# Kernel tuning notes

Measured on AMD Instinct MI355X. Metric: run time of the kernel, lower is better.

The kernel has to match this reference:

```python
import jax, jax.numpy as jnp
import numpy as np

D_MODEL = 1024
N_HEADS = 16
D_K = 64
BATCH = 2
SEQ = 2048
LN_EPS = 1e-5


def setup_inputs() -> dict:
    key = jax.random.key(0)
    ks = jax.random.split(key, 6)
    s = 1.0 / np.sqrt(D_MODEL)
    return {
        "h": jax.random.normal(ks[0], (BATCH, SEQ, D_MODEL), dtype=jnp.float32),
        "Wq": jax.random.normal(ks[1], (D_MODEL, D_MODEL), dtype=jnp.float32) * s,
        "bq": jnp.zeros((D_MODEL,), jnp.float32),
        "Wk": jax.random.normal(ks[2], (D_MODEL, D_MODEL), dtype=jnp.float32) * s,
        "bk": jnp.zeros((D_MODEL,), jnp.float32),
        "Wv": jax.random.normal(ks[3], (D_MODEL, D_MODEL), dtype=jnp.float32) * s,
        "bv": jnp.zeros((D_MODEL,), jnp.float32),
        "Wo": jax.random.normal(ks[4], (D_MODEL, D_MODEL), dtype=jnp.float32) * s,
        "bo": jnp.zeros((D_MODEL,), jnp.float32),
        "ln_w": jnp.ones((D_MODEL,), jnp.float32),
        "ln_b": jnp.zeros((D_MODEL,), jnp.float32),
    }


def _layernorm(x, w, b):
    mu = jnp.mean(x, axis=-1, keepdims=True)
    var = jnp.var(x, axis=-1, keepdims=True)
    return (x - mu) * jax.lax.rsqrt(var + LN_EPS) * w + b


def reference(h, Wq, bq, Wk, bk, Wv, bv, Wo, bo, ln_w, ln_b):
    b, s, _ = h.shape
    scale = 1.0 / np.sqrt(D_K)
    h_res = h
    hn = _layernorm(h, ln_w, ln_b)
    # Linear layers (torch convention: y = x @ W.T + b), split into heads
    q = (hn @ Wq.T + bq).reshape(b, s, N_HEADS, D_K)
    k = (hn @ Wk.T + bk).reshape(b, s, N_HEADS, D_K)
    v = (hn @ Wv.T + bv).reshape(b, s, N_HEADS, D_K)
    attn = jnp.einsum('bihd,bjhd->bhij', q, k) * scale  # [b, h, i, j]
    attn = jax.nn.softmax(attn, axis=-1)
    o = jnp.einsum('bhij,bjhd->bihd', attn, v).reshape(b, s, N_HEADS * D_K)
    out = o @ Wo.T + bo
    return out + h_res
```

## Files before the change

kernel.cpp:

```cpp
#include <hip/hip_runtime.h>
#include <cstdint>

#define D_MODEL 1024
#define N_HEADS 16
#define D_K     64
#define BATCH   2
#define SEQ     2048
#define TOKENS  (BATCH * SEQ)
#define LN_EPS  1e-5f
#define QSCALE  0.18033688011112042f

typedef __bf16 bf16x8 __attribute__((ext_vector_type(8)));
typedef float  floatx4  __attribute__((ext_vector_type(4)));
typedef float  floatx16 __attribute__((ext_vector_type(16)));
typedef unsigned uint32x2 __attribute__((ext_vector_type(2)));

__device__ __forceinline__ unsigned short f2bf(float f) {
  union { float f; unsigned u; } v; v.f = f;
  unsigned r = v.u + 0x7fffu + ((v.u >> 16) & 1u);
  return (unsigned short)(r >> 16);
}
__device__ __forceinline__ unsigned pk2bf(float hi, float lo) {
  union { float f; unsigned u; } a, b;
  a.f = hi; b.f = lo;
  return __builtin_amdgcn_perm(a.u, b.u, 0x07060302u);
}

__device__ __forceinline__ void cp16(void* lds, const void* g) {
  __builtin_amdgcn_global_load_lds(
      (__attribute__((address_space(1))) void*)g,
      (__attribute__((address_space(3))) void*)lds, 16, 0, 0);
}

__device__ __forceinline__ uint32x2 pswap(unsigned a, unsigned b) {
  return __builtin_amdgcn_permlane32_swap(a, b, false, false);
}

__global__ __launch_bounds__(256) void prep_kernel(
    const float* __restrict__ h, const float* __restrict__ w0,
    const float* __restrict__ w1, const float* __restrict__ w2,
    const float* __restrict__ w3, const float* __restrict__ lw,
    const float* __restrict__ lb, unsigned short* __restrict__ Wcat,
    unsigned short* __restrict__ hn) {
  if (blockIdx.x < 4096) {
    int wsel = blockIdx.x >> 10;
    const float* s = (wsel == 0) ? w0 : (wsel == 1) ? w1 : (wsel == 2) ? w2 : w3;
    unsigned short* d = Wcat + ((size_t)wsel << 20);
    int i = ((blockIdx.x & 1023) << 8) + threadIdx.x;
    float4 v = reinterpret_cast<const float4*>(s)[i];
    ushort4 o;
    o.x = f2bf(v.x); o.y = f2bf(v.y); o.z = f2bf(v.z); o.w = f2bf(v.w);
    reinterpret_cast<ushort4*>(d)[i] = o;
    return;
  }
  int row = blockIdx.x - 4096;
  const float* x = h + (size_t)row * D_MODEL;
  float4 v = reinterpret_cast<const float4*>(x)[threadIdx.x];
  float s  = v.x + v.y + v.z + v.w;
  float s2 = v.x * v.x + v.y * v.y + v.z * v.z + v.w * v.w;
  for (int m = 1; m < 64; m <<= 1) {
    s  += __shfl_xor(s, m);
    s2 += __shfl_xor(s2, m);
  }
  __shared__ float ls[4], ls2[4];
  int wave = threadIdx.x >> 6;
  if ((threadIdx.x & 63) == 0) { ls[wave] = s; ls2[wave] = s2; }
  __syncthreads();
  s  = ls[0] + ls[1] + ls[2] + ls[3];
  s2 = ls2[0] + ls2[1] + ls2[2] + ls2[3];
  float mu  = s * (1.0f / D_MODEL);
  float var = s2 * (1.0f / D_MODEL) - mu * mu;
  float rs  = rsqrtf(var + LN_EPS);
  float4 wv = reinterpret_cast<const float4*>(lw)[threadIdx.x];
  float4 bv = reinterpret_cast<const float4*>(lb)[threadIdx.x];
  ushort4 o;
  o.x = f2bf((v.x - mu) * rs * wv.x + bv.x);
  o.y = f2bf((v.y - mu) * rs * wv.y + bv.y);
  o.z = f2bf((v.z - mu) * rs * wv.z + bv.z);
  o.w = f2bf((v.w - mu) * rs * wv.w + bv.w);
  reinterpret_cast<ushort4*>(hn + (size_t)row * D_MODEL)[threadIdx.x] = o;
}

__global__ __launch_bounds__(512, 2) void gemm_qkv_kernel(
    const unsigned short* __restrict__ A, const unsigned short* __restrict__ Wcat,
    const float* __restrict__ bq, const float* __restrict__ bk,
    const float* __restrict__ bv,
    unsigned short* __restrict__ QK, unsigned short* __restrict__ VtG) {
  __shared__ unsigned short As[2][256 * 64];
  __shared__ unsigned short Bs[2][192 * 64];

  const int tid  = threadIdx.x;
  const int w    = tid >> 6;
  const int lane = tid & 63;
  const int l15  = lane & 15;
  const int quad = lane >> 4;
  const int sw   = l15 & 7;
  const int wrow = (w >> 1) * 64;
  const int wcol = (w & 1) * 96;

  const int flat  = blockIdx.x + (blockIdx.y << 4);
  const int swzid = ((flat & 7) << 5) + (flat >> 3);
  const int bm = (swzid >> 4) * 256;
  const int bn = (swzid & 15) * 192;

  const int srow = tid >> 3;
  const int swzc = (((tid & 7) ^ (srow & 7)) * 8);
  const unsigned short* ga = A    + (size_t)(bm + srow) * 1024 + swzc;
  const unsigned short* gb = Wcat + (size_t)(bn + srow) * 1024 + swzc;

  floatx4 acc[4][6];
#pragma unroll
  for (int i = 0; i < 4; ++i)
#pragma unroll
    for (int j = 0; j < 6; ++j) acc[i][j] = {0.f, 0.f, 0.f, 0.f};

  auto stage = [&](int k0, int b) {
    unsigned short* asl = &As[b][0] + w * 512;
    unsigned short* bsl = &Bs[b][0] + w * 512;
#pragma unroll
    for (int i = 0; i < 4; ++i) cp16(asl + i * 4096, ga + (size_t)i * 64 * 1024 + k0);
#pragma unroll
    for (int i = 0; i < 3; ++i) cp16(bsl + i * 4096, gb + (size_t)i * 64 * 1024 + k0);
  };

  stage(0, 0);

  for (int t = 0; t < 16; ++t) {
    __syncthreads();
    if (t + 1 < 16) stage((t + 1) * 64, (t + 1) & 1);
    const unsigned short* Ab = &As[t & 1][0];
    const unsigned short* Bb = &Bs[t & 1][0];
#pragma unroll
    for (int kb = 0; kb < 2; ++kb) {
      bf16x8 af[4], bfr[6];
#pragma unroll
      for (int mi = 0; mi < 4; ++mi)
        af[mi] = *reinterpret_cast<const bf16x8*>(
            Ab + (wrow + mi * 16 + l15) * 64 + (((kb * 4 + quad) ^ sw) * 8));
#pragma unroll
      for (int ni = 0; ni < 6; ++ni)
        bfr[ni] = *reinterpret_cast<const bf16x8*>(
            Bb + (wcol + ni * 16 + l15) * 64 + (((kb * 4 + quad) ^ sw) * 8));
#pragma unroll
      for (int mi = 0; mi < 4; ++mi)
#pragma unroll
        for (int ni = 0; ni < 6; ++ni)
          acc[mi][ni] = __builtin_amdgcn_mfma_f32_16x16x32_bf16(af[mi], bfr[ni], acc[mi][ni], 0, 0, 0);
    }
  }

#pragma unroll
  for (int mi = 0; mi < 4; ++mi) {
    const int row0 = bm + wrow + mi * 16 + quad * 4;
#pragma unroll
    for (int ni = 0; ni < 6; ++ni) {
      const int cb  = bn + wcol + ni * 16;
      const int col = cb + l15;
      if (cb < 1024) {
        float bb = bq[col];
#pragma unroll
        for (int r = 0; r < 4; ++r)
          QK[(size_t)(row0 + r) * 2048 + col] = f2bf((acc[mi][ni][r] + bb) * QSCALE);
      } else if (cb < 2048) {
        float bb = bk[col - 1024];
#pragma unroll
        for (int r = 0; r < 4; ++r)
          QK[(size_t)(row0 + r) * 2048 + col] = f2bf(acc[mi][ni][r] + bb);
      } else {
        int d = col - 2048;
        float bb = bv[d];
        ushort4 o;
        o.x = f2bf(acc[mi][ni][0] + bb);
        o.y = f2bf(acc[mi][ni][1] + bb);
        o.z = f2bf(acc[mi][ni][2] + bb);
        o.w = f2bf(acc[mi][ni][3] + bb);
        *reinterpret_cast<ushort4*>(VtG + (size_t)d * 4096 + row0) = o;
      }
    }
  }
}

__global__ __launch_bounds__(256) void gemm_out_kernel(
    const unsigned short* __restrict__ A, const unsigned short* __restrict__ Bt,
    const float* __restrict__ bo, const float* __restrict__ resid,
    float* __restrict__ out) {
  __shared__ unsigned short As[128 * 64];
  __shared__ unsigned short Bs[64 * 64];

  const int tid  = threadIdx.x;
  const int w    = tid >> 6;
  const int lane = tid & 63;
  const int l15  = lane & 15;
  const int quad = lane >> 4;
  const int sw   = l15 & 7;
  const int wm = (w >> 1) * 64;
  const int wn = (w & 1) * 32;
  const int bm = blockIdx.y * 128;
  const int bn = blockIdx.x * 64;

  const int srow = tid >> 3;
  const int swzc = (((tid & 7) ^ (srow & 7)) * 8);
  const unsigned short* ga = A  + (size_t)(bm + srow) * 1024 + swzc;
  const unsigned short* gb = Bt + (size_t)(bn + srow) * 1024 + swzc;
  unsigned short* asl = As + w * 512;
  unsigned short* bsl = Bs + w * 512;

  floatx4 acc[4][2];
  for (int i = 0; i < 4; ++i)
    for (int j = 0; j < 2; ++j) acc[i][j] = {0.f, 0.f, 0.f, 0.f};

  for (int k0 = 0; k0 < 1024; k0 += 64) {
#pragma unroll
    for (int i = 0; i < 4; ++i) cp16(asl + i * 2048, ga + (size_t)i * 32 * 1024 + k0);
#pragma unroll
    for (int i = 0; i < 2; ++i) cp16(bsl + i * 2048, gb + (size_t)i * 32 * 1024 + k0);
    __syncthreads();
#pragma unroll
    for (int kb = 0; kb < 2; ++kb) {
      bf16x8 af[4], bfr[2];
#pragma unroll
      for (int mi = 0; mi < 4; ++mi)
        af[mi] = *reinterpret_cast<const bf16x8*>(
            As + (wm + mi * 16 + l15) * 64 + (((kb * 4 + quad) ^ sw) * 8));
#pragma unroll
      for (int ni = 0; ni < 2; ++ni)
        bfr[ni] = *reinterpret_cast<const bf16x8*>(
            Bs + (wn + ni * 16 + l15) * 64 + (((kb * 4 + quad) ^ sw) * 8));
#pragma unroll
      for (int mi = 0; mi < 4; ++mi)
#pragma unroll
        for (int ni = 0; ni < 2; ++ni)
          acc[mi][ni] = __builtin_amdgcn_mfma_f32_16x16x32_bf16(af[mi], bfr[ni], acc[mi][ni], 0, 0, 0);
    }
    __syncthreads();
  }

#pragma unroll
  for (int mi = 0; mi < 4; ++mi)
#pragma unroll
    for (int ni = 0; ni < 2; ++ni) {
      int col = bn + wn + ni * 16 + l15;
      float bb = bo[col];
#pragma unroll
      for (int r = 0; r < 4; ++r) {
        int row = bm + wm + mi * 16 + quad * 4 + r;
        size_t idx = (size_t)row * 1024 + col;
        out[idx] = acc[mi][ni][r] + bb + resid[idx];
      }
    }
}

__global__ __launch_bounds__(512, 4) void attn_kernel(
    const unsigned short* __restrict__ QK, const unsigned short* __restrict__ VtG,
    unsigned short* __restrict__ O) {
  __shared__ unsigned short Ks[2][128 * 64];
  __shared__ unsigned short Vs[2][64 * 128];

  const int tid  = threadIdx.x;
  const int w    = tid >> 6;
  const int wq   = w & 3;
  const int kb0  = (w >> 2) * 2;
  const int lane = tid & 63;
  const int l31  = lane & 31;
  const int h    = lane >> 5;
  const int rsw  = (l31 & 7) ^ ((l31 >> 3) << 1);

  const int hh = blockIdx.x, qt = blockIdx.y, bz = blockIdx.z;
  const int tq0  = bz * SEQ + qt * 128;
  const int hoff = hh * 64;

  bf16x8 qf[4];
  {
    const unsigned short* qp =
        QK + (size_t)(tq0 + wq * 32 + l31) * 2048 + hoff + h * 8;
#pragma unroll
    for (int kd = 0; kd < 4; ++kd)
      qf[kd] = *reinterpret_cast<const bf16x8*>(qp + kd * 16);
  }

  floatx16 oacc[2];
#pragma unroll
  for (int db = 0; db < 2; ++db)
#pragma unroll
    for (int r = 0; r < 16; ++r) oacc[db][r] = 0.f;
  float lsum = 0.f;

  const unsigned short* kg = QK + 1024 + hoff
      + (size_t)(bz * SEQ + (tid >> 3)) * 2048
      + (((tid & 7) ^ ((tid >> 3) & 7) ^ ((w & 3) << 1)) * 8);
  const unsigned short* vg = VtG
      + (size_t)(hoff + (tid >> 4)) * 4096 + bz * SEQ
      + (((tid & 15) ^ ((tid >> 4) & 7) ^ (((w >> 1) & 3) << 1)) * 8);

  auto stage = [&](int kt, int b) {
    const unsigned short* kgi = kg + (size_t)(kt * 128) * 2048;
    const unsigned short* vgi = vg + kt * 128;
    unsigned short* ksl = Ks[b] + w * 512;
    unsigned short* vsl = Vs[b] + w * 512;
#pragma unroll
    for (int i = 0; i < 2; ++i) cp16(ksl + i * 4096, kgi + (size_t)(i * 64) * 2048);
#pragma unroll
    for (int i = 0; i < 2; ++i) cp16(vsl + i * 4096, vgi + (size_t)(i * 32) * 4096);
  };

  stage(0, 0);

  for (int kt = 0; kt < SEQ / 128; ++kt) {
    __syncthreads();
    if (kt + 1 < SEQ / 128) stage(kt + 1, (kt + 1) & 1);
    const unsigned short* Kb = Ks[kt & 1];
    const unsigned short* Vb = Vs[kt & 1];

    floatx16 ss[2];
#pragma unroll
    for (int kk = 0; kk < 2; ++kk)
#pragma unroll
      for (int r = 0; r < 16; ++r) ss[kk][r] = 0.f;
#pragma unroll
    for (int kk = 0; kk < 2; ++kk) {
      const int kb = kb0 + kk;
      const unsigned short* krow = Kb + (kb * 32 + l31) * 64;
#pragma unroll
      for (int kd = 0; kd < 4; ++kd) {
        bf16x8 kf = *reinterpret_cast<const bf16x8*>(
            krow + (((kd * 2 + h) ^ rsw) * 8));
        ss[kk] = __builtin_amdgcn_mfma_f32_32x32x16_bf16(kf, qf[kd], ss[kk], 0, 0, 0);
      }
    }

#pragma unroll
    for (int kk = 0; kk < 2; ++kk) {
      const int kb = kb0 + kk;
      float e[16];
      float bs = 0.f;
#pragma unroll
      for (int r = 0; r < 16; ++r) {
        e[r] = __builtin_amdgcn_exp2f(ss[kk][r]);
        bs += e[r];
      }
      {
        union { float f; unsigned u; } bu; bu.f = bs;
        uint32x2 br = pswap(bu.u, bu.u);
        union { unsigned u; float f; } b0, b1;
        b0.u = br.x; b1.u = br.y;
        bs = b0.f + b1.f;
      }
      lsum += bs;
      unsigned p[8];
#pragma unroll
      for (int i = 0; i < 8; ++i) p[i] = pk2bf(e[2 * i + 1], e[2 * i]);

#pragma unroll
      for (int sub = 0; sub < 2; ++sub) {
        uint32x2 r0 = pswap(p[sub * 4 + 0], p[sub * 4 + 2]);
        uint32x2 r1 = pswap(p[sub * 4 + 1], p[sub * 4 + 3]);
        union { unsigned u[4]; bf16x8 v; } pf;
        pf.u[0] = r0.x;
        pf.u[1] = r1.x;
        pf.u[2] = r0.y;
        pf.u[3] = r1.y;
#pragma unroll
        for (int db = 0; db < 2; ++db) {
          bf16x8 vf = *reinterpret_cast<const bf16x8*>(
              Vb + (db * 32 + l31) * 128 + (((kb * 4 + sub * 2 + h) ^ rsw) * 8));
          oacc[db] = __builtin_amdgcn_mfma_f32_32x32x16_bf16(vf, pf.v, oacc[db], 0, 0, 0);
        }
      }
    }
  }

  __syncthreads();
  float* osc = (float*)&Ks[0][0];
  float* lsc = (float*)&Vs[0][0];
  if (w >= 4) {
    float* dst = osc + ((size_t)(wq * 64 + lane) * 32);
#pragma unroll
    for (int db = 0; db < 2; ++db)
#pragma unroll
      for (int r = 0; r < 16; ++r)
        dst[(db * 16 + r + lane) & 31] = oacc[db][r];
    lsc[wq * 64 + lane] = lsum;
  }
  __syncthreads();
  if (w < 4) {
    const float* src = osc + ((size_t)(wq * 64 + lane) * 32);
    lsum += lsc[wq * 64 + lane];
#pragma unroll
    for (int db = 0; db < 2; ++db)
#pragma unroll
      for (int r = 0; r < 16; ++r)
        oacc[db][r] += src[(db * 16 + r + lane) & 31];

    float inv = 1.0f / lsum;
    unsigned short* ob = O + (size_t)(tq0 + wq * 32 + l31) * 1024 + hoff;
#pragma unroll
    for (int db = 0; db < 2; ++db)
#pragma unroll
      for (int rg = 0; rg < 4; ++rg) {
        int d0 = db * 32 + rg * 8 + h * 4;
        uint2 ov;
        ov.x = pk2bf(oacc[db][rg * 4 + 1] * inv, oacc[db][rg * 4 + 0] * inv);
        ov.y = pk2bf(oacc[db][rg * 4 + 3] * inv, oacc[db][rg * 4 + 2] * inv);
        *reinterpret_cast<uint2*>(ob + d0) = ov;
      }
  }
}

extern "C" void kernel_launch(void* const* d_in, const int* in_sizes, int n_in,
                              void* d_out, int out_size, void* d_ws, size_t ws_size,
                              hipStream_t stream) {
  const float* h    = (const float*)d_in[0];
  const float* Wq   = (const float*)d_in[1];
  const float* bq   = (const float*)d_in[2];
  const float* Wk   = (const float*)d_in[3];
  const float* bk   = (const float*)d_in[4];
  const float* Wv   = (const float*)d_in[5];
  const float* bv   = (const float*)d_in[6];
  const float* Wo   = (const float*)d_in[7];
  const float* bo   = (const float*)d_in[8];
  const float* ln_w = (const float*)d_in[9];
  const float* ln_b = (const float*)d_in[10];
  float* out = (float*)d_out;

  unsigned short* ws = (unsigned short*)d_ws;
  const size_t WSZ = (size_t)1 << 20;
  unsigned short* Wcat = ws;
  unsigned short* hn   = Wcat + 4 * WSZ;
  unsigned short* QKb  = hn + (size_t)TOKENS * D_MODEL;
  unsigned short* VtG  = QKb + (size_t)TOKENS * 2048;
  unsigned short* Obuf = VtG + (size_t)D_MODEL * TOKENS;

  prep_kernel<<<8192, 256, 0, stream>>>(h, Wq, Wk, Wv, Wo, ln_w, ln_b, Wcat, hn);

  gemm_qkv_kernel<<<dim3(16, 16), 512, 0, stream>>>(hn, Wcat, bq, bk, bv, QKb, VtG);

  attn_kernel<<<dim3(N_HEADS, SEQ / 128, BATCH), 512, 0, stream>>>(QKb, VtG, Obuf);

  gemm_out_kernel<<<dim3(16, 32), 256, 0, stream>>>(Obuf, Wcat + 3 * WSZ, bo, h, out);
}
```

Baseline: 197.2 us.

## Double attention block to 16 waves, one key sub-block per wave

The attention kernel now launches 1024 threads per block, and each of the 16 waves handles one 32-key sub-block instead of two. This halves per-wave serial work and adds waves for latency hiding. Each thread issues one 16-byte copy per tile for K and one for V. The final reduction across the four key-split wave groups is staged through shared memory in two phases (one per output half), which adds extra barriers and shared-memory traffic. The launch bound declares 8 blocks per SM at 1024 threads, which is unrealistic and may make the compiler tighten the register limit.

```diff
diff --git a/kernel.cpp b/kernel.cpp
--- a/kernel.cpp
+++ b/kernel.cpp
@@ -250,16 +250,15 @@
     }
 }
 
-__global__ __launch_bounds__(512, 4) void attn_kernel(
+__global__ __launch_bounds__(1024, 8) void attn_kernel(
     const unsigned short* __restrict__ QK, const unsigned short* __restrict__ VtG,
     unsigned short* __restrict__ O) {
-  __shared__ unsigned short Ks[2][128 * 64];
-  __shared__ unsigned short Vs[2][64 * 128];
+  __shared__ unsigned short smem[4 * 8192];
 
   const int tid  = threadIdx.x;
   const int w    = tid >> 6;
   const int wq   = w & 3;
-  const int kb0  = (w >> 2) * 2;
+  const int kb   = w >> 2;
   const int lane = tid & 63;
   const int l31  = lane & 31;
   const int h    = lane >> 5;
@@ -293,14 +292,8 @@
       + (((tid & 15) ^ ((tid >> 4) & 7) ^ (((w >> 1) & 3) << 1)) * 8);
 
   auto stage = [&](int kt, int b) {
-    const unsigned short* kgi = kg + (size_t)(kt * 128) * 2048;
-    const unsigned short* vgi = vg + kt * 128;
-    unsigned short* ksl = Ks[b] + w * 512;
-    unsigned short* vsl = Vs[b] + w * 512;
-#pragma unroll
-    for (int i = 0; i < 2; ++i) cp16(ksl + i * 4096, kgi + (size_t)(i * 64) * 2048);
-#pragma unroll
-    for (int i = 0; i < 2; ++i) cp16(vsl + i * 4096, vgi + (size_t)(i * 32) * 4096);
+    cp16(smem + b * 8192 + w * 512, kg + (size_t)(kt * 128) * 2048);
+    cp16(smem + 16384 + b * 8192 + w * 512, vg + kt * 128);
   };
 
   stage(0, 0);
@@ -308,89 +301,94 @@
   for (int kt = 0; kt < SEQ / 128; ++kt) {
     __syncthreads();
     if (kt + 1 < SEQ / 128) stage(kt + 1, (kt + 1) & 1);
-    const unsigned short* Kb = Ks[kt & 1];
-    const unsigned short* Vb = Vs[kt & 1];
-
-    floatx16 ss[2];
-#pragma unroll
-    for (int kk = 0; kk < 2; ++kk)
-#pragma unroll
-      for (int r = 0; r < 16; ++r) ss[kk][r] = 0.f;
-#pragma unroll
-    for (int kk = 0; kk < 2; ++kk) {
-      const int kb = kb0 + kk;
-      const unsigned short* krow = Kb + (kb * 32 + l31) * 64;
-#pragma unroll
-      for (int kd = 0; kd < 4; ++kd) {
-        bf16x8 kf = *reinterpret_cast<const bf16x8*>(
-            krow + (((kd * 2 + h) ^ rsw) * 8));
-        ss[kk] = __builtin_amdgcn_mfma_f32_32x32x16_bf16(kf, qf[kd], ss[kk], 0, 0, 0);
+    const unsigned short* Kb = smem + (kt & 1) * 8192;
+    const unsigned short* Vb = smem + 16384 + (kt & 1) * 8192;
+
+    floatx16 ss;
+#pragma unroll
+    for (int r = 0; r < 16; ++r) ss[r] = 0.f;
+    const unsigned short* krow = Kb + (kb * 32 + l31) * 64;
+#pragma unroll
+    for (int kd = 0; kd < 4; ++kd) {
+      bf16x8 kf = *reinterpret_cast<const bf16x8*>(
+          krow + (((kd * 2 + h) ^ rsw) * 8));
+      ss = __builtin_amdgcn_mfma_f32_32x32x16_bf16(kf, qf[kd], ss, 0, 0, 0);
+    }
+
+    float e[16];
+#pragma unroll
+    for (int r = 0; r < 16; ++r) e[r] = __builtin_amdgcn_exp2f(ss[r]);
+    float s0 = e[0] + e[1],   s1 = e[2] + e[3],   s2 = e[4] + e[5],
+          s3 = e[6] + e[7],   s4 = e[8] + e[9],   s5 = e[10] + e[11],
+          s6 = e[12] + e[13], s7s = e[14] + e[15];
+    float t0 = s0 + s1, t1 = s2 + s3, t2 = s4 + s5, t3 = s6 + s7s;
+    float bs = (t0 + t1) + (t2 + t3);
+    {
+      union { float f; unsigned u; } bu; bu.f = bs;
+      uint32x2 br = pswap(bu.u, bu.u);
+      union { unsigned u; float f; } b0, b1;
+      b0.u = br.x; b1.u = br.y;
+      bs = b0.f + b1.f;
+    }
+    lsum += bs;
+    unsigned p[8];
+#pragma unroll
+    for (int i = 0; i < 8; ++i) p[i] = pk2bf(e[2 * i + 1], e[2 * i]);
+
+#pragma unroll
+    for (int sub = 0; sub < 2; ++sub) {
+      uint32x2 r0 = pswap(p[sub * 4 + 0], p[sub * 4 + 2]);
+      uint32x2 r1 = pswap(p[sub * 4 + 1], p[sub * 4 + 3]);
+      union { unsigned u[4]; bf16x8 v; } pf;
+      pf.u[0] = r0.x;
+      pf.u[1] = r1.x;
+      pf.u[2] = r0.y;
+      pf.u[3] = r1.y;
+#pragma unroll
+      for (int db = 0; db < 2; ++db) {
+        bf16x8 vf = *reinterpret_cast<const bf16x8*>(
+            Vb + (db * 32 + l31) * 128 + (((kb * 4 + sub * 2 + h) ^ rsw) * 8));
+        oacc[db] = __builtin_amdgcn_mfma_f32_32x32x16_bf16(vf, pf.v, oacc[db], 0, 0, 0);
       }
     }
-
-#pragma unroll
-    for (int kk = 0; kk < 2; ++kk) {
-      const int kb = kb0 + kk;
-      float e[16];
-      float bs = 0.f;
-#pragma unroll
-      for (int r = 0; r < 16; ++r) {
-        e[r] = __builtin_amdgcn_exp2f(ss[kk][r]);
-        bs += e[r];
-      }
-      {
-        union { float f; unsigned u; } bu; bu.f = bs;
-        uint32x2 br = pswap(bu.u, bu.u);
-        union { unsigned u; float f; } b0, b1;
-        b0.u = br.x; b1.u = br.y;
-        bs = b0.f + b1.f;
-      }
-      lsum += bs;
-      unsigned p[8];
-#pragma unroll
-      for (int i = 0; i < 8; ++i) p[i] = pk2bf(e[2 * i + 1], e[2 * i]);
-
-#pragma unroll
-      for (int sub = 0; sub < 2; ++sub) {
-        uint32x2 r0 = pswap(p[sub * 4 + 0], p[sub * 4 + 2]);
-        uint32x2 r1 = pswap(p[sub * 4 + 1], p[sub * 4 + 3]);
-        union { unsigned u[4]; bf16x8 v; } pf;
-        pf.u[0] = r0.x;
-        pf.u[1] = r1.x;
-        pf.u[2] = r0.y;
-        pf.u[3] = r1.y;
-#pragma unroll
-        for (int db = 0; db < 2; ++db) {
-          bf16x8 vf = *reinterpret_cast<const bf16x8*>(
-              Vb + (db * 32 + l31) * 128 + (((kb * 4 + sub * 2 + h) ^ rsw) * 8));
-          oacc[db] = __builtin_amdgcn_mfma_f32_32x32x16_bf16(vf, pf.v, oacc[db], 0, 0, 0);
-        }
-      }
-    }
-  }
+  }
+
+  float* osc = (float*)smem;
+  float* lsc = (float*)(smem + 24576);
+  const int slot = (kb - 1) * 256 + wq * 64 + lane;
+  const int rslot = wq * 64 + lane;
 
   __syncthreads();
-  float* osc = (float*)&Ks[0][0];
-  float* lsc = (float*)&Vs[0][0];
-  if (w >= 4) {
-    float* dst = osc + ((size_t)(wq * 64 + lane) * 32);
-#pragma unroll
-    for (int db = 0; db < 2; ++db)
-#pragma unroll
-      for (int r = 0; r < 16; ++r)
-        dst[(db * 16 + r + lane) & 31] = oacc[db][r];
-    lsc[wq * 64 + lane] = lsum;
+  if (kb > 0) {
+    float* dst = osc + (size_t)slot * 16;
+#pragma unroll
+    for (int r = 0; r < 16; ++r) dst[(r + lane) & 15] = oacc[0][r];
+    lsc[slot] = lsum;
   }
   __syncthreads();
-  if (w < 4) {
-    const float* src = osc + ((size_t)(wq * 64 + lane) * 32);
-    lsum += lsc[wq * 64 + lane];
-#pragma unroll
-    for (int db = 0; db < 2; ++db)
-#pragma unroll
-      for (int r = 0; r < 16; ++r)
-        oacc[db][r] += src[(db * 16 + r + lane) & 31];
-
+  if (kb == 0) {
+    lsum += lsc[rslot] + lsc[256 + rslot] + lsc[512 + rslot];
+#pragma unroll
+    for (int gi = 0; gi < 3; ++gi) {
+      const float* src = osc + (size_t)(gi * 256 + rslot) * 16;
+#pragma unroll
+      for (int r = 0; r < 16; ++r) oacc[0][r] += src[(r + lane) & 15];
+    }
+  }
+  __syncthreads();
+  if (kb > 0) {
+    float* dst = osc + (size_t)slot * 16;
+#pragma unroll
+    for (int r = 0; r < 16; ++r) dst[(r + lane) & 15] = oacc[1][r];
+  }
+  __syncthreads();
+  if (kb == 0) {
+#pragma unroll
+    for (int gi = 0; gi < 3; ++gi) {
+      const float* src = osc + (size_t)(gi * 256 + rslot) * 16;
+#pragma unroll
+      for (int r = 0; r < 16; ++r) oacc[1][r] += src[(r + lane) & 15];
+    }
     float inv = 1.0f / lsum;
     unsigned short* ob = O + (size_t)(tq0 + wq * 32 + l31) * 1024 + hoff;
 #pragma unroll
@@ -434,7 +432,7 @@
 
   gemm_qkv_kernel<<<dim3(16, 16), 512, 0, stream>>>(hn, Wcat, bq, bk, bv, QKb, VtG);
 
-  attn_kernel<<<dim3(N_HEADS, SEQ / 128, BATCH), 512, 0, stream>>>(QKb, VtG, Obuf);
+  attn_kernel<<<dim3(N_HEADS, SEQ / 128, BATCH), 1024, 0, stream>>>(QKb, VtG, Obuf);
 
   gemm_out_kernel<<<dim3(16, 32), 256, 0, stream>>>(Obuf, Wcat + 3 * WSZ, bo, h, out);
 }
```

Result: slower. 430.6 us (+118.4%).
